# Performance work log

Hardware: AMD Instinct MI355X
Metric: run time of the kernel (lower is better)

Reference implementation:

```python
import jax, jax.numpy as jnp
import numpy as np

N = 65536        # total points across batch
NS = 16          # nsample (kNN neighbors)
D = 64           # d_model
FF = 64          # dim_feedforward width
CIN = 16         # input feature channels
EPS = 1e-5       # BatchNorm eps


def _bn_relu(x, g, b):
    # BatchNorm1d in training mode: per-channel stats over (N, L); x: (N, C, L)
    m = x.mean(axis=(0, 2), keepdims=True)
    v = x.var(axis=(0, 2), keepdims=True)
    return jax.nn.relu((x - m) * jax.lax.rsqrt(v + EPS) * g[None, :, None] + b[None, :, None])


def _dknn_layer(xyz, feats, knn_idx, knn_empty,
                wq, bq, wk, bk, w1, g1, b1, w2, g2, b2, wo, go, bo):
    # nhead = 1 -> single head uses the full d_model split
    Q = feats @ wq + bq                        # (N, D)
    K = feats @ wk + bk                        # (N, D)
    Kx = jnp.concatenate([K, xyz], axis=1)     # use_xyz=True -> (N, D+3)
    Qx = jnp.concatenate([Q, xyz], axis=1)     # (N, D+3)
    Kg = jnp.transpose(Kx[knn_idx], (0, 2, 1))  # irregular gather -> (N, D+3, NS)
    Qe = Qx[:, :, None]                        # (N, D+3, 1)
    x = jnp.concatenate([Kg - Qe, jnp.broadcast_to(Qe, Kg.shape)], axis=1)  # (N, 2*(D+3), NS)
    x = jnp.where(knn_empty[:, None, None], 0.0, x)   # empty-ball masking
    x = _bn_relu(jnp.einsum('ncs,cf->nfs', x, w1), g1, b1)  # Conv1d k=1 == channel matmul
    x = _bn_relu(jnp.einsum('ncs,cf->nfs', x, w2), g2, b2)
    x = jnp.max(x, axis=2, keepdims=True)      # max-pool over neighbors -> (N, FF, 1)
    x = _bn_relu(jnp.einsum('ncs,cf->nfs', x, wo), go, bo)  # out_conv
    return x[:, :, 0]                          # (N, D)


def setup_inputs() -> dict:
    key = jax.random.key(0)
    ks = jax.random.split(key, 16)
    inp = {
        'src_xyz': jax.random.normal(ks[0], (N, 3), jnp.float32) * 20.0,
        'src_feats': jax.random.normal(ks[1], (N, CIN), jnp.float32),
        'knn_idx': jax.random.randint(ks[2], (N, NS), 0, N, jnp.int32),
        'knn_empty': jax.random.randint(ks[3], (N,), 0, 20, jnp.int32) == 0,
    }
    k = 4
    cin = CIN
    for i in range(2):
        s = 1.0 / np.sqrt(cin)
        inp[f'l{i}_wq'] = jax.random.normal(ks[k], (cin, D), jnp.float32) * s; k += 1
        inp[f'l{i}_bq'] = jnp.zeros((D,), jnp.float32)
        inp[f'l{i}_wk'] = jax.random.normal(ks[k], (cin, D), jnp.float32) * s; k += 1
        inp[f'l{i}_bk'] = jnp.zeros((D,), jnp.float32)
        c = 2 * (D + 3)
        inp[f'l{i}_w1'] = jax.random.normal(ks[k], (c, FF), jnp.float32) * np.sqrt(2.0 / c); k += 1
        inp[f'l{i}_g1'] = jnp.ones((FF,), jnp.float32)
        inp[f'l{i}_b1'] = jnp.zeros((FF,), jnp.float32)
        inp[f'l{i}_w2'] = jax.random.normal(ks[k], (FF, FF), jnp.float32) * np.sqrt(2.0 / FF); k += 1
        inp[f'l{i}_g2'] = jnp.ones((FF,), jnp.float32)
        inp[f'l{i}_b2'] = jnp.zeros((FF,), jnp.float32)
        inp[f'l{i}_wo'] = jax.random.normal(ks[k], (FF, D), jnp.float32) * np.sqrt(2.0 / FF); k += 1
        inp[f'l{i}_go'] = jnp.ones((D,), jnp.float32)
        inp[f'l{i}_bo'] = jnp.zeros((D,), jnp.float32)
        cin = D
    return inp


def reference(src_xyz, src_feats, knn_idx, knn_empty,
              l0_wq, l0_bq, l0_wk, l0_bk, l0_w1, l0_g1, l0_b1, l0_w2, l0_g2, l0_b2, l0_wo, l0_go, l0_bo,
              l1_wq, l1_bq, l1_wk, l1_bk, l1_w1, l1_g1, l1_b1, l1_w2, l1_g2, l1_b2, l1_wo, l1_go, l1_bo):
    f = _dknn_layer(src_xyz, src_feats, knn_idx, knn_empty,
                    l0_wq, l0_bq, l0_wk, l0_bk, l0_w1, l0_g1, l0_b1, l0_w2, l0_g2, l0_b2, l0_wo, l0_go, l0_bo)
    f = _dknn_layer(src_xyz, f, knn_idx, knn_empty,
                    l1_wq, l1_bq, l1_wk, l1_bk, l1_w1, l1_g1, l1_b1, l1_w2, l1_g2, l1_b2, l1_wo, l1_go, l1_bo)
    return f
```

## Files before the change

### kernel.cpp

```cpp
#include <hip/hip_runtime.h>
#include <cstdint>

#define NPTS 65536
#define NS 16
#define EPSV 1e-5f

typedef __attribute__((ext_vector_type(8))) short bf16x8;
typedef __attribute__((ext_vector_type(8))) unsigned short u16x8;
typedef __attribute__((ext_vector_type(4))) float f32x4;
typedef __attribute__((ext_vector_type(4))) unsigned int u32x4;
union FragU { u32x4 u; bf16x8 h; };

#define SUM1 0
#define SSQ1 64
#define SUM2 128
#define SSQ2 192
#define SUM3 256
#define SSQ3 320
#define WKAOF 0
#define WQBAOF 4096
#define BKAOF 8192
#define BQBAOF 8256
#define WFOLD_FLOATS 8320

__device__ __forceinline__ void split2(float e0, float e1, unsigned int& hi, unsigned int& lo) {
    unsigned int u0 = __float_as_uint(e0), u1 = __float_as_uint(e1);
    hi = __builtin_amdgcn_perm(u1, u0, 0x07060302u);
    float l0f = e0 - __uint_as_float(u0 & 0xFFFF0000u);
    float l1f = e1 - __uint_as_float(u1 & 0xFFFF0000u);
    lo = __builtin_amdgcn_perm(__float_as_uint(l1f), __float_as_uint(l0f), 0x07060302u);
}

__device__ __forceinline__ unsigned short f2bf(float x) {
    unsigned int u = __float_as_uint(x);
    u += 0x7FFFu + ((u >> 16) & 1u);
    return (unsigned short)(u >> 16);
}
__device__ __forceinline__ float bf2f(unsigned short h) {
    return __uint_as_float(((unsigned int)h) << 16);
}

__global__ void k_mask(const uint32_t* emp32, uint8_t* mask) {
    int bad = 0;
    for (int w = threadIdx.x; w < 1024; w += 256) bad |= (emp32[w] > 1u) ? 1 : 0;
    __shared__ int sbad[4];
    unsigned long long b = __ballot(bad != 0);
    if ((threadIdx.x & 63) == 0) sbad[threadIdx.x >> 6] = (b != 0ull) ? 1 : 0;
    __syncthreads();
    int flag = sbad[0] | sbad[1] | sbad[2] | sbad[3];
    int i = blockIdx.x * 256 + threadIdx.x;
    uint8_t mv;
    if (flag) mv = (((const uint8_t*)emp32)[i] != 0);
    else      mv = (emp32[i] != 0u);
    mask[i] = mv;
}

__global__ void k0(const float* wq, const float* bq, const float* wk, const float* bk,
                   const float* w1, float* wfold, int cin) {
    int f = threadIdx.x;
    int c = blockIdx.x;
    float a = 0.f, q = 0.f;
    for (int d = 0; d < 64; d++) {
        float A  = w1[d*64 + f];
        float Bm = w1[(67+d)*64 + f] - A;
        a = fmaf(wk[c*64 + d], A,  a);
        q = fmaf(wq[c*64 + d], Bm, q);
    }
    wfold[WKAOF  + c*64 + f] = a;
    wfold[WQBAOF + c*64 + f] = q;
    if (c == 0) {
        float ba = 0.f, bqv = 0.f;
        for (int d = 0; d < 64; d++) {
            float A  = w1[d*64 + f];
            float Bm = w1[(67+d)*64 + f] - A;
            ba  = fmaf(bk[d], A,  ba);
            bqv = fmaf(bq[d], Bm, bqv);
        }
        wfold[BKAOF  + f] = ba;
        wfold[BQBAOF + f] = bqv;
    }
}

template<int CIN, bool PREBN>
__global__ void __launch_bounds__(256) k1m(const float* __restrict__ feats, const float* __restrict__ xyz,
                    const float* __restrict__ w1, const float* __restrict__ wfold,
                    const float* __restrict__ statsPrev, const float* __restrict__ goP,
                    const float* __restrict__ boP,
                    unsigned short* __restrict__ KAb, float* __restrict__ QBA) {
    const int l = threadIdx.x & 63;
    const int wv = threadIdx.x >> 6;
    const int sidx = l & 15;
    const int g = l >> 4;
    const int col = sidx;
    constexpr int NT = (CIN == 64) ? 2 : 1;

    unsigned int bh[NT][2][4], bl[NT][2][4];
    #pragma unroll
    for (int t = 0; t < NT; t++)
    #pragma unroll
    for (int fl = 0; fl < 2; fl++) {
        int f128 = (wv*2 + fl)*16 + col;
        const float* W = (f128 < 64) ? (wfold + WKAOF) : (wfold + WQBAOF);
        int f = (f128 < 64) ? f128 : f128 - 64;
        #pragma unroll
        for (int r = 0; r < 4; r++) {
            int c0 = t*32 + g*8 + 2*r;
            float e0 = 0.f, e1 = 0.f;
            if (CIN == 64 || g < 2) {
                e0 = W[c0*64 + f];
                e1 = W[(c0+1)*64 + f];
            }
            split2(e0, e1, bh[t][fl][r], bl[t][fl][r]);
        }
    }
    unsigned int xbh[2][4], xbl[2][4];
    float biasf[2];
    #pragma unroll
    for (int fl = 0; fl < 2; fl++) {
        int f128 = (wv*2 + fl)*16 + col;
        float A0, A1, A2;
        if (f128 < 64) {
            A0 = w1[64*64 + f128]; A1 = w1[65*64 + f128]; A2 = w1[66*64 + f128];
            biasf[fl] = wfold[BKAOF + f128];
        } else {
            int f = f128 - 64;
            A0 = w1[131*64 + f] - w1[64*64 + f];
            A1 = w1[132*64 + f] - w1[65*64 + f];
            A2 = w1[133*64 + f] - w1[66*64 + f];
            biasf[fl] = wfold[BQBAOF + f];
        }
        split2(A0, A1, xbh[fl][0], xbl[fl][0]);
        split2(A2, 0.f, xbh[fl][1], xbl[fl][1]);
        xbh[fl][2] = 0; xbh[fl][3] = 0; xbl[fl][2] = 0; xbl[fl][3] = 0;
    }
    float scP[NT*8], shP[NT*8];
    if (PREBN) {
        const float invN = 1.0f / (float)NPTS;
        #pragma unroll
        for (int t = 0; t < NT; t++)
        #pragma unroll
        for (int i = 0; i < 8; i++) {
            int c = t*32 + g*8 + i;
            float m = statsPrev[SUM3 + c] * invN;
            float v = fmaxf(statsPrev[SSQ3 + c] * invN - m*m, 0.0f);
            float s = goP[c] * rsqrtf(v + EPSV);
            scP[t*8+i] = s;
            shP[t*8+i] = fmaf(-m, s, boP[c]);
        }
    }

    for (int tile = blockIdx.x; tile < NPTS/16; tile += gridDim.x) {
        int p = tile*16 + sidx;
        unsigned int ahu[NT][4], alu[NT][4];
        #pragma unroll
        for (int t = 0; t < NT; t++) {
            float xv[8];
            if (CIN == 64) {
                f32x4 a0 = *(const f32x4*)(feats + (size_t)p*64 + t*32 + g*8);
                f32x4 a1 = *(const f32x4*)(feats + (size_t)p*64 + t*32 + g*8 + 4);
                #pragma unroll
                for (int i = 0; i < 4; i++) { xv[i] = a0[i]; xv[4+i] = a1[i]; }
                if (PREBN) {
                    #pragma unroll
                    for (int i = 0; i < 8; i++)
                        xv[i] = fmaxf(fmaf(scP[t*8+i], xv[i], shP[t*8+i]), 0.0f);
                }
            } else {
                if (g < 2) {
                    f32x4 a0 = *(const f32x4*)(feats + (size_t)p*16 + g*8);
                    f32x4 a1 = *(const f32x4*)(feats + (size_t)p*16 + g*8 + 4);
                    #pragma unroll
                    for (int i = 0; i < 4; i++) { xv[i] = a0[i]; xv[4+i] = a1[i]; }
                } else {
                    #pragma unroll
                    for (int i = 0; i < 8; i++) xv[i] = 0.f;
                }
            }
            #pragma unroll
            for (int r = 0; r < 4; r++) split2(xv[2*r], xv[2*r+1], ahu[t][r], alu[t][r]);
        }
        unsigned int xah[4] = {0,0,0,0}, xal[4] = {0,0,0,0};
        if (g == 0) {
            float x0 = xyz[p*3], x1 = xyz[p*3+1], x2 = xyz[p*3+2];
            split2(x0, x1, xah[0], xal[0]);
            split2(x2, 0.f, xah[1], xal[1]);
        }
        f32x4 acc[2];
        #pragma unroll
        for (int fl = 0; fl < 2; fl++)
            acc[fl] = (f32x4){biasf[fl], biasf[fl], biasf[fl], biasf[fl]};
        #pragma unroll
        for (int t = 0; t < NT; t++) {
            FragU ah, al;
            ah.u = (u32x4){ahu[t][0], ahu[t][1], ahu[t][2], ahu[t][3]};
            al.u = (u32x4){alu[t][0], alu[t][1], alu[t][2], alu[t][3]};
            #pragma unroll
            for (int fl = 0; fl < 2; fl++) {
                FragU Bh, Bl;
                Bh.u = (u32x4){bh[t][fl][0], bh[t][fl][1], bh[t][fl][2], bh[t][fl][3]};
                Bl.u = (u32x4){bl[t][fl][0], bl[t][fl][1], bl[t][fl][2], bl[t][fl][3]};
                acc[fl] = __builtin_amdgcn_mfma_f32_16x16x32_bf16(ah.h, Bh.h, acc[fl], 0, 0, 0);
                acc[fl] = __builtin_amdgcn_mfma_f32_16x16x32_bf16(ah.h, Bl.h, acc[fl], 0, 0, 0);
                acc[fl] = __builtin_amdgcn_mfma_f32_16x16x32_bf16(al.h, Bh.h, acc[fl], 0, 0, 0);
            }
        }
        {
            FragU ah, al;
            ah.u = (u32x4){xah[0], xah[1], xah[2], xah[3]};
            al.u = (u32x4){xal[0], xal[1], xal[2], xal[3]};
            #pragma unroll
            for (int fl = 0; fl < 2; fl++) {
                FragU Bh, Bl;
                Bh.u = (u32x4){xbh[fl][0], xbh[fl][1], xbh[fl][2], xbh[fl][3]};
                Bl.u = (u32x4){xbl[fl][0], xbl[fl][1], xbl[fl][2], xbl[fl][3]};
                acc[fl] = __builtin_amdgcn_mfma_f32_16x16x32_bf16(ah.h, Bh.h, acc[fl], 0, 0, 0);
                acc[fl] = __builtin_amdgcn_mfma_f32_16x16x32_bf16(ah.h, Bl.h, acc[fl], 0, 0, 0);
                acc[fl] = __builtin_amdgcn_mfma_f32_16x16x32_bf16(al.h, Bh.h, acc[fl], 0, 0, 0);
            }
        }
        #pragma unroll
        for (int fl = 0; fl < 2; fl++) {
            int f128 = (wv*2 + fl)*16 + col;
            #pragma unroll
            for (int r = 0; r < 4; r++) {
                int po = tile*16 + g*4 + r;
                float v = acc[fl][r];
                if (f128 < 64) KAb[(size_t)po*64 + f128] = f2bf(v);
                else           QBA[(size_t)po*64 + (f128-64)] = v;
            }
        }
    }
}

__global__ void __launch_bounds__(256) k2(const unsigned short* __restrict__ KAb, const float* __restrict__ QBA,
                   const int* __restrict__ knn, const uint8_t* __restrict__ mask, float* stats) {
    const int l = threadIdx.x & 63;
    const int wv = threadIdx.x >> 6;
    const int s = l & 15;
    const int g = l >> 4;
    float s0[16], s1[16];
    #pragma unroll
    for (int i = 0; i < 16; i++) { s0[i] = 0.f; s1[i] = 0.f; }

    const int STR = gridDim.x * 16;
    for (int n0 = blockIdx.x * 16 + wv*4; n0 < NPTS; n0 += STR) {
        bool msk[4];
        u16x8 ka[4][2];
        #pragma unroll
        for (int u = 0; u < 4; u++) {
            int n = n0 + u;
            msk[u] = (mask[n] != 0);
            if (!msk[u]) {
                int j = knn[n*16 + s];
                const unsigned short* kp = KAb + (size_t)j*64;
                ka[u][0] = *(const u16x8*)(kp + g*8);
                ka[u][1] = *(const u16x8*)(kp + 32 + g*8);
            }
        }
        #pragma unroll
        for (int u = 0; u < 4; u++) {
            if (msk[u]) continue;
            int n = n0 + u;
            const float* qp = QBA + (size_t)n*64;
            f32x4 q0 = *(const f32x4*)(qp + g*8);
            f32x4 q1 = *(const f32x4*)(qp + g*8 + 4);
            f32x4 q2 = *(const f32x4*)(qp + 32 + g*8);
            f32x4 q3 = *(const f32x4*)(qp + 32 + g*8 + 4);
            #pragma unroll
            for (int t = 0; t < 2; t++)
            #pragma unroll
            for (int i = 0; i < 8; i++) {
                float kf = bf2f(ka[u][t][i]);
                float qv = t ? ((i < 4) ? q2[i] : q3[i-4])
                             : ((i < 4) ? q0[i] : q1[i-4]);
                float y = kf + qv;
                s0[t*8+i] += y;
                s1[t*8+i] = fmaf(y, y, s1[t*8+i]);
            }
        }
    }
    #pragma unroll
    for (int i = 0; i < 16; i++) {
        #pragma unroll
        for (int d = 1; d < 16; d <<= 1) {
            s0[i] += __shfl_xor(s0[i], d, 64);
            s1[i] += __shfl_xor(s1[i], d, 64);
        }
    }
    __shared__ float r0[4][64], r1[4][64];
    if (s == 0) {
        #pragma unroll
        for (int t = 0; t < 2; t++)
        #pragma unroll
        for (int i = 0; i < 8; i++) {
            int c = t*32 + g*8 + i;
            r0[wv][c] = s0[t*8+i];
            r1[wv][c] = s1[t*8+i];
        }
    }
    __syncthreads();
    int tid = threadIdx.x;
    if (tid < 64) {
        atomicAdd(&stats[SUM1 + tid], r0[0][tid]+r0[1][tid]+r0[2][tid]+r0[3][tid]);
        atomicAdd(&stats[SSQ1 + tid], r1[0][tid]+r1[1][tid]+r1[2][tid]+r1[3][tid]);
    }
}

__global__ void __launch_bounds__(256) k4(const unsigned short* __restrict__ KAb, const float* __restrict__ QBA,
                   const int* __restrict__ knn, const uint8_t* __restrict__ mask,
                   const float* __restrict__ w2, const float* __restrict__ g1, const float* __restrict__ b1,
                   float* stats, float* __restrict__ y2max, float* __restrict__ y2min) {
    const int l    = threadIdx.x & 63;
    const int wv   = threadIdx.x >> 6;
    const int sidx = l & 15;
    const int g    = l >> 4;
    const int col  = sidx;

    float sc1v[16], sh1v[16];
    const float inv = 1.0f / ((float)NPTS * (float)NS);
    #pragma unroll
    for (int t = 0; t < 2; t++)
    #pragma unroll
    for (int i = 0; i < 8; i++) {
        int c = t*32 + g*8 + i;
        float m = stats[SUM1 + c] * inv;
        float v = fmaxf(stats[SSQ1 + c] * inv - m*m, 0.0f);
        float s = g1[c] * rsqrtf(v + EPSV);
        sc1v[t*8+i] = s;
        sh1v[t*8+i] = fmaf(-m, s, b1[c]);
    }

    unsigned int whu[2][4][4], wlu[2][4][4];
    #pragma unroll
    for (int t = 0; t < 2; t++)
    #pragma unroll
    for (int ft = 0; ft < 4; ft++)
    #pragma unroll
    for (int r = 0; r < 4; r++) {
        int k0i = t*32 + g*8 + 2*r;
        float e0 = w2[k0i*64 + ft*16 + col];
        float e1 = w2[(k0i+1)*64 + ft*16 + col];
        split2(e0, e1, whu[t][ft][r], wlu[t][ft][r]);
    }

    float s0t[4] = {0.f,0.f,0.f,0.f};
    float s1t[4] = {0.f,0.f,0.f,0.f};

    const int STR = gridDim.x * 16;
    for (int n0 = blockIdx.x * 16 + wv*4; n0 < NPTS; n0 += STR) {
        bool msk[4];
        u16x8 ka[4][2];
        #pragma unroll
        for (int u = 0; u < 4; u++) {
            int n = n0 + u;
            msk[u] = (mask[n] != 0);
            int j = knn[n*16 + sidx];
            const unsigned short* kp = KAb + (size_t)j*64;
            ka[u][0] = *(const u16x8*)(kp + g*8);
            ka[u][1] = *(const u16x8*)(kp + 32 + g*8);
        }
        #pragma unroll
        for (int u = 0; u < 4; u++) {
            int n = n0 + u;
            bool masked = msk[u];
            const float* qp = QBA + (size_t)n*64;
            f32x4 q0 = *(const f32x4*)(qp + g*8);
            f32x4 q1 = *(const f32x4*)(qp + g*8 + 4);
            f32x4 q2 = *(const f32x4*)(qp + 32 + g*8);
            f32x4 q3 = *(const f32x4*)(qp + 32 + g*8 + 4);

            float x[16];
            #pragma unroll
            for (int t = 0; t < 2; t++)
            #pragma unroll
            for (int i = 0; i < 8; i++) {
                float kf = bf2f(ka[u][t][i]);
                float qv = t ? ((i < 4) ? q2[i] : q3[i-4])
                             : ((i < 4) ? q0[i] : q1[i-4]);
                float y = masked ? 0.f : (kf + qv);
                x[t*8+i] = fmaxf(fmaf(sc1v[t*8+i], y, sh1v[t*8+i]), 0.0f);
            }

            unsigned int ahu[2][4], alu[2][4];
            #pragma unroll
            for (int t = 0; t < 2; t++)
            #pragma unroll
            for (int r = 0; r < 4; r++)
                split2(x[t*8 + 2*r], x[t*8 + 2*r + 1], ahu[t][r], alu[t][r]);

            f32x4 acc[4];
            #pragma unroll
            for (int ft = 0; ft < 4; ft++) acc[ft] = (f32x4){0.f,0.f,0.f,0.f};

            #pragma unroll
            for (int t = 0; t < 2; t++) {
                FragU ah, al;
                ah.u = (u32x4){ahu[t][0], ahu[t][1], ahu[t][2], ahu[t][3]};
                al.u = (u32x4){alu[t][0], alu[t][1], alu[t][2], alu[t][3]};
                #pragma unroll
                for (int ft = 0; ft < 4; ft++) {
                    FragU bhf, blf;
                    bhf.u = (u32x4){whu[t][ft][0], whu[t][ft][1], whu[t][ft][2], whu[t][ft][3]};
                    blf.u = (u32x4){wlu[t][ft][0], wlu[t][ft][1], wlu[t][ft][2], wlu[t][ft][3]};
                    acc[ft] = __builtin_amdgcn_mfma_f32_16x16x32_bf16(ah.h, bhf.h, acc[ft], 0, 0, 0);
                    acc[ft] = __builtin_amdgcn_mfma_f32_16x16x32_bf16(ah.h, blf.h, acc[ft], 0, 0, 0);
                    acc[ft] = __builtin_amdgcn_mfma_f32_16x16x32_bf16(al.h, bhf.h, acc[ft], 0, 0, 0);
                }
            }

            float tmax[4], tmin[4];
            #pragma unroll
            for (int ft = 0; ft < 4; ft++) {
                f32x4 d = acc[ft];
                float lmax = fmaxf(fmaxf(d[0], d[1]), fmaxf(d[2], d[3]));
                float lmin = fminf(fminf(d[0], d[1]), fminf(d[2], d[3]));
                s0t[ft] += (d[0] + d[1]) + (d[2] + d[3]);
                s1t[ft] += fmaf(d[0],d[0], fmaf(d[1],d[1], fmaf(d[2],d[2], d[3]*d[3])));
                lmax = fmaxf(lmax, __shfl_xor(lmax, 16, 64));
                lmax = fmaxf(lmax, __shfl_xor(lmax, 32, 64));
                lmin = fminf(lmin, __shfl_xor(lmin, 16, 64));
                lmin = fminf(lmin, __shfl_xor(lmin, 32, 64));
                tmax[ft] = lmax; tmin[ft] = lmin;
            }
            float mx = (g==0) ? tmax[0] : (g==1) ? tmax[1] : (g==2) ? tmax[2] : tmax[3];
            float mn = (g==0) ? tmin[0] : (g==1) ? tmin[1] : (g==2) ? tmin[2] : tmin[3];
            y2max[(size_t)n*64 + l] = mx;
            y2min[(size_t)n*64 + l] = mn;
        }
    }

    #pragma unroll
    for (int ft = 0; ft < 4; ft++) {
        s0t[ft] += __shfl_xor(s0t[ft], 16, 64);
        s0t[ft] += __shfl_xor(s0t[ft], 32, 64);
        s1t[ft] += __shfl_xor(s1t[ft], 16, 64);
        s1t[ft] += __shfl_xor(s1t[ft], 32, 64);
    }
    float myS0 = (g==0) ? s0t[0] : (g==1) ? s0t[1] : (g==2) ? s0t[2] : s0t[3];
    float myS1 = (g==0) ? s1t[0] : (g==1) ? s1t[1] : (g==2) ? s1t[2] : s1t[3];
    __shared__ float red[8][64];
    red[wv][l] = myS0;
    red[4+wv][l] = myS1;
    __syncthreads();
    if (wv == 0) {
        atomicAdd(&stats[SUM2 + l], red[0][l]+red[1][l]+red[2][l]+red[3][l]);
        atomicAdd(&stats[SSQ2 + l], red[4][l]+red[5][l]+red[6][l]+red[7][l]);
    }
}

__global__ void __launch_bounds__(256) k5m(const float* __restrict__ y2max, const float* __restrict__ y2min,
                    const float* __restrict__ wo, const float* __restrict__ g2, const float* __restrict__ b2,
                    float* stats, float* __restrict__ y3) {
    const int l = threadIdx.x & 63;
    const int wv = threadIdx.x >> 6;
    const int sidx = l & 15;
    const int g = l >> 4;
    const int ft = wv;

    unsigned int bh[2][4], bl[2][4];
    #pragma unroll
    for (int t = 0; t < 2; t++)
    #pragma unroll
    for (int r = 0; r < 4; r++) {
        int c0 = t*32 + g*8 + 2*r;
        split2(wo[c0*64 + ft*16 + sidx], wo[(c0+1)*64 + ft*16 + sidx], bh[t][r], bl[t][r]);
    }
    float sc2v[16], sh2v[16];
    const float inv = 1.0f / ((float)NPTS * (float)NS);
    #pragma unroll
    for (int t = 0; t < 2; t++)
    #pragma unroll
    for (int i = 0; i < 8; i++) {
        int c = t*32 + g*8 + i;
        float m = stats[SUM2 + c] * inv;
        float v = fmaxf(stats[SSQ2 + c] * inv - m*m, 0.0f);
        float s = g2[c] * rsqrtf(v + EPSV);
        sc2v[t*8+i] = s;
        sh2v[t*8+i] = fmaf(-m, s, b2[c]);
    }
    float s0a = 0.f, s1a = 0.f;
    for (int tile = blockIdx.x; tile < NPTS/16; tile += gridDim.x) {
        int p = tile*16 + sidx;
        unsigned int ahu[2][4], alu[2][4];
        #pragma unroll
        for (int t = 0; t < 2; t++) {
            f32x4 mx0 = *(const f32x4*)(y2max + (size_t)p*64 + t*32 + g*8);
            f32x4 mx1 = *(const f32x4*)(y2max + (size_t)p*64 + t*32 + g*8 + 4);
            f32x4 mn0 = *(const f32x4*)(y2min + (size_t)p*64 + t*32 + g*8);
            f32x4 mn1 = *(const f32x4*)(y2min + (size_t)p*64 + t*32 + g*8 + 4);
            float mval[8];
            #pragma unroll
            for (int i = 0; i < 4; i++) {
                float sc = sc2v[t*8+i];
                float pre = (sc >= 0.f) ? mx0[i] : mn0[i];
                mval[i] = fmaxf(fmaf(sc, pre, sh2v[t*8+i]), 0.0f);
                float sc2 = sc2v[t*8+4+i];
                float pre2 = (sc2 >= 0.f) ? mx1[i] : mn1[i];
                mval[4+i] = fmaxf(fmaf(sc2, pre2, sh2v[t*8+4+i]), 0.0f);
            }
            #pragma unroll
            for (int r = 0; r < 4; r++) split2(mval[2*r], mval[2*r+1], ahu[t][r], alu[t][r]);
        }
        f32x4 acc = (f32x4){0.f,0.f,0.f,0.f};
        #pragma unroll
        for (int t = 0; t < 2; t++) {
            FragU ah, al, Bh, Bl;
            ah.u = (u32x4){ahu[t][0], ahu[t][1], ahu[t][2], ahu[t][3]};
            al.u = (u32x4){alu[t][0], alu[t][1], alu[t][2], alu[t][3]};
            Bh.u = (u32x4){bh[t][0], bh[t][1], bh[t][2], bh[t][3]};
            Bl.u = (u32x4){bl[t][0], bl[t][1], bl[t][2], bl[t][3]};
            acc = __builtin_amdgcn_mfma_f32_16x16x32_bf16(ah.h, Bh.h, acc, 0, 0, 0);
            acc = __builtin_amdgcn_mfma_f32_16x16x32_bf16(ah.h, Bl.h, acc, 0, 0, 0);
            acc = __builtin_amdgcn_mfma_f32_16x16x32_bf16(al.h, Bh.h, acc, 0, 0, 0);
        }
        #pragma unroll
        for (int r = 0; r < 4; r++) {
            int po = tile*16 + g*4 + r;
            float v = acc[r];
            y3[(size_t)po*64 + ft*16 + sidx] = v;
            s0a += v;
            s1a = fmaf(v, v, s1a);
        }
    }
    s0a += __shfl_xor(s0a, 16, 64); s0a += __shfl_xor(s0a, 32, 64);
    s1a += __shfl_xor(s1a, 16, 64); s1a += __shfl_xor(s1a, 32, 64);
    __shared__ float r0[64], r1[64];
    if (l < 16) { r0[wv*16 + sidx] = s0a; r1[wv*16 + sidx] = s1a; }
    __syncthreads();
    int tid = threadIdx.x;
    if (tid < 64) {
        atomicAdd(&stats[SUM3 + tid], r0[tid]);
        atomicAdd(&stats[SSQ3 + tid], r1[tid]);
    }
}

__global__ void k6(float* y3, const float* stats, const float* go, const float* bo) {
    int i = blockIdx.x * 256 + threadIdx.x;
    int f = i & 63;
    const float inv = 1.0f / (float)NPTS;
    float m = stats[SUM3 + f] * inv;
    float v = fmaxf(stats[SSQ3 + f] * inv - m*m, 0.0f);
    float s = go[f] * rsqrtf(v + EPSV);
    float sh = fmaf(-m, s, bo[f]);
    y3[i] = fmaxf(fmaf(s, y3[i], sh), 0.0f);
}

extern "C" void kernel_launch(void* const* d_in, const int* in_sizes, int n_in,
                              void* d_out, int out_size, void* d_ws, size_t ws_size,
                              hipStream_t stream) {
    const float* xyz    = (const float*)d_in[0];
    const float* feats0 = (const float*)d_in[1];
    const int*   knn    = (const int*)d_in[2];
    const void*  empty  = d_in[3];
    float* ws = (float*)d_ws;
    const size_t N64 = (size_t)NPTS * 64;
    unsigned short* KAb = (unsigned short*)ws;
    float* QBA   = ws + N64;
    float* Y2MAX = ws + 2*N64;
    float* Y2MIN = ws + 3*N64;
    float* stats = ws + 4*N64;
    float* wfold = stats + 1024;
    uint8_t* mask = (uint8_t*)(wfold + WFOLD_FLOATS);
    float* out = (float*)d_out;

    hipMemsetAsync(stats, 0, 1024 * sizeof(float), stream);
    k_mask<<<NPTS/256, 256, 0, stream>>>((const uint32_t*)empty, mask);

    const float* const* p0 = (const float* const*)(d_in + 4);
    const float* const* p1 = (const float* const*)(d_in + 4 + 13);

    {
        const float* const* p = p0;
        float* sl = stats;
        k0<<<16, 64, 0, stream>>>(p[0], p[1], p[2], p[3], p[4], wfold, 16);
        k1m<16, false><<<1024, 256, 0, stream>>>(feats0, xyz, p[4], wfold,
                                                 sl, p[11], p[12], KAb, QBA);
        k2<<<2048, 256, 0, stream>>>(KAb, QBA, knn, mask, sl);
        k4<<<2048, 256, 0, stream>>>(KAb, QBA, knn, mask, p[7], p[5], p[6], sl, Y2MAX, Y2MIN);
        k5m<<<2048, 256, 0, stream>>>(Y2MAX, Y2MIN, p[10], p[8], p[9], sl, out);
    }
    {
        const float* const* p = p1;
        float* sl = stats + 512;
        k0<<<64, 64, 0, stream>>>(p[0], p[1], p[2], p[3], p[4], wfold, 64);
        k1m<64, true><<<1024, 256, 0, stream>>>(out, xyz, p[4], wfold,
                                                stats, p0[11], p0[12], KAb, QBA);
        k2<<<2048, 256, 0, stream>>>(KAb, QBA, knn, mask, sl);
        k4<<<2048, 256, 0, stream>>>(KAb, QBA, knn, mask, p[7], p[5], p[6], sl, Y2MAX, Y2MIN);
        k5m<<<2048, 256, 0, stream>>>(Y2MAX, Y2MIN, p[10], p[8], p[9], sl, out);
        k6<<<NPTS*64/256, 256, 0, stream>>>(out, sl, p[11], p[12]);
    }
}
```

Measured before the change: 581.9 us.

## Stage W2 split fragments in LDS, halve per-wave unroll, skip min reads

In k4, the hi/lo bf16 split of w2 was held in 64 registers per lane. It is now written once to shared memory by the first wave and read back per MFMA, and the per-wave point unroll drops from 4 to 2. Together these are meant to cut VGPR pressure and raise occupancy for the latency-bound neighbour gather, at the cost of extra LDS reads. In k5m, a wave-wide ballot checks whether any BN scale is negative and skips loading y2min when none is, removing half of that kernel's input traffic.

```diff
diff --git a/kernel.cpp b/kernel.cpp
--- a/kernel.cpp
+++ b/kernel.cpp
@@ -316,6 +316,9 @@
     const int g    = l >> 4;
     const int col  = sidx;
 
+    __shared__ unsigned int wlds[16*64*4];
+    __shared__ float red[8][64];
+
     float sc1v[16], sh1v[16];
     const float inv = 1.0f / ((float)NPTS * (float)NS);
     #pragma unroll
@@ -330,28 +333,36 @@
         sh1v[t*8+i] = fmaf(-m, s, b1[c]);
     }
 
-    unsigned int whu[2][4][4], wlu[2][4][4];
-    #pragma unroll
-    for (int t = 0; t < 2; t++)
-    #pragma unroll
-    for (int ft = 0; ft < 4; ft++)
-    #pragma unroll
-    for (int r = 0; r < 4; r++) {
-        int k0i = t*32 + g*8 + 2*r;
-        float e0 = w2[k0i*64 + ft*16 + col];
-        float e1 = w2[(k0i+1)*64 + ft*16 + col];
-        split2(e0, e1, whu[t][ft][r], wlu[t][ft][r]);
-    }
+    if (threadIdx.x < 64) {
+        #pragma unroll
+        for (int t = 0; t < 2; t++)
+        #pragma unroll
+        for (int ft = 0; ft < 4; ft++) {
+            unsigned int wh[4], wl[4];
+            #pragma unroll
+            for (int r = 0; r < 4; r++) {
+                int k0i = t*32 + g*8 + 2*r;
+                split2(w2[k0i*64 + ft*16 + col], w2[(k0i+1)*64 + ft*16 + col], wh[r], wl[r]);
+            }
+            int idxh = t*8 + ft*2, idxl = idxh + 1;
+            #pragma unroll
+            for (int r = 0; r < 4; r++) {
+                wlds[(idxh*64 + l)*4 + r] = wh[r];
+                wlds[(idxl*64 + l)*4 + r] = wl[r];
+            }
+        }
+    }
+    __syncthreads();
 
     float s0t[4] = {0.f,0.f,0.f,0.f};
     float s1t[4] = {0.f,0.f,0.f,0.f};
 
-    const int STR = gridDim.x * 16;
-    for (int n0 = blockIdx.x * 16 + wv*4; n0 < NPTS; n0 += STR) {
-        bool msk[4];
-        u16x8 ka[4][2];
-        #pragma unroll
-        for (int u = 0; u < 4; u++) {
+    const int STR = gridDim.x * 8;
+    for (int n0 = blockIdx.x * 8 + wv*2; n0 < NPTS; n0 += STR) {
+        bool msk[2];
+        u16x8 ka[2][2];
+        #pragma unroll
+        for (int u = 0; u < 2; u++) {
             int n = n0 + u;
             msk[u] = (mask[n] != 0);
             int j = knn[n*16 + sidx];
@@ -360,7 +371,7 @@
             ka[u][1] = *(const u16x8*)(kp + 32 + g*8);
         }
         #pragma unroll
-        for (int u = 0; u < 4; u++) {
+        for (int u = 0; u < 2; u++) {
             int n = n0 + u;
             bool masked = msk[u];
             const float* qp = QBA + (size_t)n*64;
@@ -399,12 +410,16 @@
                 al.u = (u32x4){alu[t][0], alu[t][1], alu[t][2], alu[t][3]};
                 #pragma unroll
                 for (int ft = 0; ft < 4; ft++) {
-                    FragU bhf, blf;
-                    bhf.u = (u32x4){whu[t][ft][0], whu[t][ft][1], whu[t][ft][2], whu[t][ft][3]};
-                    blf.u = (u32x4){wlu[t][ft][0], wlu[t][ft][1], wlu[t][ft][2], wlu[t][ft][3]};
-                    acc[ft] = __builtin_amdgcn_mfma_f32_16x16x32_bf16(ah.h, bhf.h, acc[ft], 0, 0, 0);
-                    acc[ft] = __builtin_amdgcn_mfma_f32_16x16x32_bf16(ah.h, blf.h, acc[ft], 0, 0, 0);
-                    acc[ft] = __builtin_amdgcn_mfma_f32_16x16x32_bf16(al.h, bhf.h, acc[ft], 0, 0, 0);
+                    unsigned int offh = ((t*8 + ft*2)*64 + l)*4;
+                    unsigned int offl = offh + 256;
+                    asm volatile("" : "+v"(offh));
+                    asm volatile("" : "+v"(offl));
+                    FragU Bh, Bl;
+                    Bh.u = *(const u32x4*)&wlds[offh];
+                    Bl.u = *(const u32x4*)&wlds[offl];
+                    acc[ft] = __builtin_amdgcn_mfma_f32_16x16x32_bf16(ah.h, Bh.h, acc[ft], 0, 0, 0);
+                    acc[ft] = __builtin_amdgcn_mfma_f32_16x16x32_bf16(ah.h, Bl.h, acc[ft], 0, 0, 0);
+                    acc[ft] = __builtin_amdgcn_mfma_f32_16x16x32_bf16(al.h, Bh.h, acc[ft], 0, 0, 0);
                 }
             }
 
@@ -438,7 +453,6 @@
     }
     float myS0 = (g==0) ? s0t[0] : (g==1) ? s0t[1] : (g==2) ? s0t[2] : s0t[3];
     float myS1 = (g==0) ? s1t[0] : (g==1) ? s1t[1] : (g==2) ? s1t[2] : s1t[3];
-    __shared__ float red[8][64];
     red[wv][l] = myS0;
     red[4+wv][l] = myS1;
     __syncthreads();
@@ -467,6 +481,7 @@
     }
     float sc2v[16], sh2v[16];
     const float inv = 1.0f / ((float)NPTS * (float)NS);
+    int anyneg = 0;
     #pragma unroll
     for (int t = 0; t < 2; t++)
     #pragma unroll
@@ -477,7 +492,10 @@
         float s = g2[c] * rsqrtf(v + EPSV);
         sc2v[t*8+i] = s;
         sh2v[t*8+i] = fmaf(-m, s, b2[c]);
-    }
+        anyneg |= (s < 0.0f) ? 1 : 0;
+    }
+    const bool need_mn = (__ballot(anyneg != 0) != 0ull);
+
     float s0a = 0.f, s1a = 0.f;
     for (int tile = blockIdx.x; tile < NPTS/16; tile += gridDim.x) {
         int p = tile*16 + sidx;
@@ -486,8 +504,11 @@
         for (int t = 0; t < 2; t++) {
             f32x4 mx0 = *(const f32x4*)(y2max + (size_t)p*64 + t*32 + g*8);
             f32x4 mx1 = *(const f32x4*)(y2max + (size_t)p*64 + t*32 + g*8 + 4);
-            f32x4 mn0 = *(const f32x4*)(y2min + (size_t)p*64 + t*32 + g*8);
-            f32x4 mn1 = *(const f32x4*)(y2min + (size_t)p*64 + t*32 + g*8 + 4);
+            f32x4 mn0 = mx0, mn1 = mx1;
+            if (need_mn) {
+                mn0 = *(const f32x4*)(y2min + (size_t)p*64 + t*32 + g*8);
+                mn1 = *(const f32x4*)(y2min + (size_t)p*64 + t*32 + g*8 + 4);
+            }
             float mval[8];
             #pragma unroll
             for (int i = 0; i < 4; i++) {
```

Measured after the change: 629.6 us. 1.08x slower.

## Pre-fold BN1 scale into K/Q tables and skip min-buffer reads

Applied to the files above, without the earlier changes.

Adds a pass (k3) that applies the first BatchNorm scale to the bf16 K table and the scale plus shift to the Q table, so k4 only computes relu(k+q) per neighbor element instead of an affine op. Masked rows use a precomputed relu(shift). k4 now processes 2 points per wave per iteration instead of 4. k5m skips loading the per-channel min buffer when no BN2 scale is negative. The price is an extra elementwise pass over K and Q, one more bf16 rounding applied after scaling, and a wave-uniform branch in k5m.

```diff
diff --git a/kernel.cpp b/kernel.cpp
--- a/kernel.cpp
+++ b/kernel.cpp
@@ -306,6 +306,37 @@
     }
 }
 
+__global__ void __launch_bounds__(256) k3(unsigned short* KAb, float* QBA,
+                   const float* __restrict__ stats, const float* __restrict__ g1,
+                   const float* __restrict__ b1) {
+    int t = blockIdx.x * 256 + threadIdx.x;
+    int n = t >> 3, c8 = (t & 7) * 8;
+    const float inv = 1.0f / ((float)NPTS * (float)NS);
+    float sc[8], sh[8];
+    #pragma unroll
+    for (int i = 0; i < 8; i++) {
+        int c = c8 + i;
+        float m = stats[SUM1 + c] * inv;
+        float v = fmaxf(stats[SSQ1 + c] * inv - m*m, 0.0f);
+        float s = g1[c] * rsqrtf(v + EPSV);
+        sc[i] = s;
+        sh[i] = fmaf(-m, s, b1[c]);
+    }
+    u16x8 ka = *(const u16x8*)(KAb + (size_t)n*64 + c8);
+    #pragma unroll
+    for (int i = 0; i < 8; i++) ka[i] = f2bf(sc[i] * bf2f(ka[i]));
+    *(u16x8*)(KAb + (size_t)n*64 + c8) = ka;
+    f32x4 qa = *(const f32x4*)(QBA + (size_t)n*64 + c8);
+    f32x4 qb = *(const f32x4*)(QBA + (size_t)n*64 + c8 + 4);
+    #pragma unroll
+    for (int i = 0; i < 4; i++) {
+        qa[i] = fmaf(sc[i],   qa[i], sh[i]);
+        qb[i] = fmaf(sc[4+i], qb[i], sh[4+i]);
+    }
+    *(f32x4*)(QBA + (size_t)n*64 + c8)     = qa;
+    *(f32x4*)(QBA + (size_t)n*64 + c8 + 4) = qb;
+}
+
 __global__ void __launch_bounds__(256) k4(const unsigned short* __restrict__ KAb, const float* __restrict__ QBA,
                    const int* __restrict__ knn, const uint8_t* __restrict__ mask,
                    const float* __restrict__ w2, const float* __restrict__ g1, const float* __restrict__ b1,
@@ -316,7 +347,7 @@
     const int g    = l >> 4;
     const int col  = sidx;
 
-    float sc1v[16], sh1v[16];
+    float xm[16];
     const float inv = 1.0f / ((float)NPTS * (float)NS);
     #pragma unroll
     for (int t = 0; t < 2; t++)
@@ -326,8 +357,7 @@
         float m = stats[SUM1 + c] * inv;
         float v = fmaxf(stats[SSQ1 + c] * inv - m*m, 0.0f);
         float s = g1[c] * rsqrtf(v + EPSV);
-        sc1v[t*8+i] = s;
-        sh1v[t*8+i] = fmaf(-m, s, b1[c]);
+        xm[t*8+i] = fmaxf(fmaf(-m, s, b1[c]), 0.0f);
     }
 
     unsigned int whu[2][4][4], wlu[2][4][4];
@@ -346,12 +376,12 @@
     float s0t[4] = {0.f,0.f,0.f,0.f};
     float s1t[4] = {0.f,0.f,0.f,0.f};
 
-    const int STR = gridDim.x * 16;
-    for (int n0 = blockIdx.x * 16 + wv*4; n0 < NPTS; n0 += STR) {
-        bool msk[4];
-        u16x8 ka[4][2];
-        #pragma unroll
-        for (int u = 0; u < 4; u++) {
+    const int STR = gridDim.x * 8;
+    for (int n0 = blockIdx.x * 8 + wv*2; n0 < NPTS; n0 += STR) {
+        bool msk[2];
+        u16x8 ka[2][2];
+        #pragma unroll
+        for (int u = 0; u < 2; u++) {
             int n = n0 + u;
             msk[u] = (mask[n] != 0);
             int j = knn[n*16 + sidx];
@@ -360,7 +390,7 @@
             ka[u][1] = *(const u16x8*)(kp + 32 + g*8);
         }
         #pragma unroll
-        for (int u = 0; u < 4; u++) {
+        for (int u = 0; u < 2; u++) {
             int n = n0 + u;
             bool masked = msk[u];
             const float* qp = QBA + (size_t)n*64;
@@ -377,8 +407,7 @@
                 float kf = bf2f(ka[u][t][i]);
                 float qv = t ? ((i < 4) ? q2[i] : q3[i-4])
                              : ((i < 4) ? q0[i] : q1[i-4]);
-                float y = masked ? 0.f : (kf + qv);
-                x[t*8+i] = fmaxf(fmaf(sc1v[t*8+i], y, sh1v[t*8+i]), 0.0f);
+                x[t*8+i] = masked ? xm[t*8+i] : fmaxf(kf + qv, 0.0f);
             }
 
             unsigned int ahu[2][4], alu[2][4];
@@ -467,6 +496,7 @@
     }
     float sc2v[16], sh2v[16];
     const float inv = 1.0f / ((float)NPTS * (float)NS);
+    int anyneg = 0;
     #pragma unroll
     for (int t = 0; t < 2; t++)
     #pragma unroll
@@ -477,7 +507,10 @@
         float s = g2[c] * rsqrtf(v + EPSV);
         sc2v[t*8+i] = s;
         sh2v[t*8+i] = fmaf(-m, s, b2[c]);
-    }
+        anyneg |= (s < 0.0f) ? 1 : 0;
+    }
+    const bool need_mn = (__ballot(anyneg != 0) != 0ull);
+
     float s0a = 0.f, s1a = 0.f;
     for (int tile = blockIdx.x; tile < NPTS/16; tile += gridDim.x) {
         int p = tile*16 + sidx;
@@ -486,8 +519,11 @@
         for (int t = 0; t < 2; t++) {
             f32x4 mx0 = *(const f32x4*)(y2max + (size_t)p*64 + t*32 + g*8);
             f32x4 mx1 = *(const f32x4*)(y2max + (size_t)p*64 + t*32 + g*8 + 4);
-            f32x4 mn0 = *(const f32x4*)(y2min + (size_t)p*64 + t*32 + g*8);
-            f32x4 mn1 = *(const f32x4*)(y2min + (size_t)p*64 + t*32 + g*8 + 4);
+            f32x4 mn0 = mx0, mn1 = mx1;
+            if (need_mn) {
+                mn0 = *(const f32x4*)(y2min + (size_t)p*64 + t*32 + g*8);
+                mn1 = *(const f32x4*)(y2min + (size_t)p*64 + t*32 + g*8 + 4);
+            }
             float mval[8];
             #pragma unroll
             for (int i = 0; i < 4; i++) {
@@ -576,6 +612,7 @@
         k1m<16, false><<<1024, 256, 0, stream>>>(feats0, xyz, p[4], wfold,
                                                  sl, p[11], p[12], KAb, QBA);
         k2<<<2048, 256, 0, stream>>>(KAb, QBA, knn, mask, sl);
+        k3<<<NPTS*8/256, 256, 0, stream>>>(KAb, QBA, sl, p[5], p[6]);
         k4<<<2048, 256, 0, stream>>>(KAb, QBA, knn, mask, p[7], p[5], p[6], sl, Y2MAX, Y2MIN);
         k5m<<<2048, 256, 0, stream>>>(Y2MAX, Y2MIN, p[10], p[8], p[9], sl, out);
     }
@@ -586,6 +623,7 @@
         k1m<64, true><<<1024, 256, 0, stream>>>(out, xyz, p[4], wfold,
                                                 stats, p0[11], p0[12], KAb, QBA);
         k2<<<2048, 256, 0, stream>>>(KAb, QBA, knn, mask, sl);
+        k3<<<NPTS*8/256, 256, 0, stream>>>(KAb, QBA, sl, p[5], p[6]);
         k4<<<2048, 256, 0, stream>>>(KAb, QBA, knn, mask, p[7], p[5], p[6], sl, Y2MAX, Y2MIN);
         k5m<<<2048, 256, 0, stream>>>(Y2MAX, Y2MIN, p[10], p[8], p[9], sl, out);
         k6<<<NPTS*64/256, 256, 0, stream>>>(out, sl, p[11], p[12]);
```

New measurement: 598.4 us. 2.8% more time.
